# Kernel tuning notes

Hardware: AMD Instinct MI355X
Metric: run time of the kernel (lower is better)

## Reference

```python
import jax, jax.numpy as jnp
import numpy as np

B, S, H = 1, 2048, 4096
NH, NKV, HD = 32, 8, 128
N_REP = NH // NKV
SCALING = HD ** -0.5
ROPE_THETA = 10000.0
NEG_INF = -1e9


def setup_inputs() -> dict:
    key = jax.random.key(0)
    ks = jax.random.split(key, 5)
    hidden_states = jax.random.normal(ks[0], (B, S, H), dtype=jnp.float32)
    # torch nn.Linear weights are [out_features, in_features]
    wq = jax.random.normal(ks[1], (NH * HD, H), dtype=jnp.float32) * 0.02
    wk = jax.random.normal(ks[2], (NKV * HD, H), dtype=jnp.float32) * 0.02
    wv = jax.random.normal(ks[3], (NKV * HD, H), dtype=jnp.float32) * 0.02
    wo = jax.random.normal(ks[4], (NH * HD, H), dtype=jnp.float32).T * 0.02  # [H, NH*HD] -> store as [out,in]=[H,4096]
    wo = jnp.asarray(wo)
    # RoPE tables: [1, S, HD]
    inv_freq = 1.0 / (ROPE_THETA ** (jnp.arange(0, HD, 2, dtype=jnp.float32) / HD))
    pos = jnp.arange(S, dtype=jnp.float32)
    freqs = pos[:, None] * inv_freq[None, :]            # [S, HD/2]
    emb = jnp.concatenate([freqs, freqs], axis=-1)      # [S, HD]
    cos = jnp.cos(emb)[None]
    sin = jnp.sin(emb)[None]
    # additive causal mask [1, 1, S, S]
    causal = jnp.tril(jnp.ones((S, S), dtype=bool))
    attn_mask = jnp.where(causal, 0.0, NEG_INF).astype(jnp.float32)[None, None]
    return {"hidden_states": hidden_states, "wq": wq, "wk": wk, "wv": wv,
            "wo": wo, "cos": cos, "sin": sin, "attn_mask": attn_mask}


def rotate_half(x):
    x1, x2 = jnp.split(x, 2, axis=-1)
    return jnp.concatenate([-x2, x1], axis=-1)


def reference(hidden_states, wq, wk, wv, wo, cos, sin, attn_mask):
    b, s, _ = hidden_states.shape
    # projections (x @ W.T), reshape to [B, heads, S, HD]
    q = (hidden_states @ wq.T).reshape(b, s, NH, HD).transpose(0, 2, 1, 3)
    k = (hidden_states @ wk.T).reshape(b, s, NKV, HD).transpose(0, 2, 1, 3)
    v = (hidden_states @ wv.T).reshape(b, s, NKV, HD).transpose(0, 2, 1, 3)
    # RoPE (unsqueeze_dim=1)
    c = cos[:, None]  # [1,1,S,HD]
    sn = sin[:, None]
    q = q * c + rotate_half(q) * sn
    k = k * c + rotate_half(k) * sn
    # GQA head repeat
    k = jnp.repeat(k, N_REP, axis=1)  # [B, NH, S, HD]
    v = jnp.repeat(v, N_REP, axis=1)
    # eager attention
    scores = jnp.einsum('bhqd,bhkd->bhqk', q, k) * SCALING + attn_mask[:, :, :, :s]
    attn_weights = jax.nn.softmax(scores.astype(jnp.float32), axis=-1).astype(q.dtype)
    attn_out = jnp.einsum('bhqk,bhkd->bhqd', attn_weights, v)
    attn_out = attn_out.transpose(0, 2, 1, 3).reshape(b, s, NH * HD)
    out = attn_out @ wo.T
    return out, attn_weights
```

## Files before the change

### kernel.cpp

```cpp
#include <hip/hip_runtime.h>
#include <cstdint>
#include <cstddef>


#define SEQ 2048
#define HID 4096
#define NH_ 32
#define NKV_ 8
#define HD_ 128
#define KDIM_KV 1024
#define SCALING 0.08838834764831843f

typedef __bf16 bf16;
typedef __attribute__((ext_vector_type(8))) __bf16 bf16x8;
typedef __attribute__((ext_vector_type(4))) float f32x4;

__device__ __forceinline__ unsigned short f2bf(float f) {
  __bf16 h = (__bf16)f;
  return __builtin_bit_cast(unsigned short, h);
}
__device__ __forceinline__ float bf2f(unsigned short u) {
  unsigned int x = ((unsigned int)u) << 16;
  return __builtin_bit_cast(float, x);
}

__device__ __forceinline__ void async16(const void* g, void* l) {
  __builtin_amdgcn_global_load_lds(
      (const __attribute__((address_space(1))) unsigned int*)g,
      (__attribute__((address_space(3))) unsigned int*)l, 16, 0, 0);
}

__global__ __launch_bounds__(256) void cvt_kernel(const float* __restrict__ src,
                                                  bf16* __restrict__ dst, int n4) {
  int i = blockIdx.x * 256 + threadIdx.x;
  if (i >= n4) return;
  float4 v = ((const float4*)src)[i];
  union { unsigned short u[4]; uint2 vv; } pk;
  pk.u[0] = f2bf(v.x); pk.u[1] = f2bf(v.y);
  pk.u[2] = f2bf(v.z); pk.u[3] = f2bf(v.w);
  ((uint2*)dst)[i] = pk.vv;
}

__device__ __forceinline__ void gemm_mainloop(const char* Ab, const char* Bb,
                                              int K, char* smem, int tid,
                                              f32x4 (&acc)[4][4]) {
  const int wave = tid >> 6, lane = tid & 63;
  const int quad = lane >> 4, l16 = lane & 15;
  const int wm = wave >> 1, wn = wave & 1;
  bf16* As = (bf16*)smem;
  bf16* Bs = As + 128 * 32;

  const f32x4 fz = {0.f, 0.f, 0.f, 0.f};
#pragma unroll
  for (int i = 0; i < 4; i++)
#pragma unroll
    for (int j = 0; j < 4; j++) acc[i][j] = fz;

  const int o0 = (wave * 2 + 0) * 1024 + lane * 16;
  const int o1 = (wave * 2 + 1) * 1024 + lane * 16;
  const int rA0 = o0 >> 6, cA0 = o0 & 63;
  const int rA1 = o1 >> 6, cA1 = o1 & 63;

  for (int k0 = 0; k0 < K; k0 += 32) {
    __syncthreads();
    const size_t kb = (size_t)k0 * 2;
    async16(Ab + (size_t)rA0 * 8192 + kb + cA0, (char*)As + (wave * 2 + 0) * 1024);
    async16(Ab + (size_t)rA1 * 8192 + kb + cA1, (char*)As + (wave * 2 + 1) * 1024);
    async16(Bb + (size_t)rA0 * 8192 + kb + cA0, (char*)Bs + (wave * 2 + 0) * 1024);
    async16(Bb + (size_t)rA1 * 8192 + kb + cA1, (char*)Bs + (wave * 2 + 1) * 1024);
    __syncthreads();

    bf16x8 af[4], bfr[4];
#pragma unroll
    for (int i = 0; i < 4; i++)
      af[i] = *(const bf16x8*)(As + (size_t)(wm * 64 + i * 16 + l16) * 32 + quad * 8);
#pragma unroll
    for (int j = 0; j < 4; j++)
      bfr[j] = *(const bf16x8*)(Bs + (size_t)(wn * 64 + j * 16 + l16) * 32 + quad * 8);
#pragma unroll
    for (int i = 0; i < 4; i++)
#pragma unroll
      for (int j = 0; j < 4; j++)
        acc[i][j] = __builtin_amdgcn_mfma_f32_16x16x32_bf16(af[i], bfr[j], acc[i][j], 0, 0, 0);
  }
}

__global__ __launch_bounds__(256) void qkv_gemm(
    const bf16* __restrict__ A,
    const bf16* __restrict__ Wq,
    const bf16* __restrict__ Wk,
    const bf16* __restrict__ Wv,
    const float* __restrict__ cosp,
    const float* __restrict__ sinp,
    bf16* __restrict__ qout,
    bf16* __restrict__ kout,
    bf16* __restrict__ vtout)
{
  const int mi = blockIdx.x, nt = blockIdx.y;
  const int tid = threadIdx.x;
  const int wave = tid >> 6, lane = tid & 63;
  const int quad = lane >> 4, l16 = lane & 15;
  const int wm = wave >> 1, wn = wave & 1;

  const bf16* Bp; int nb;
  if (nt < 32)      { Bp = Wq; nb = nt; }
  else if (nt < 40) { Bp = Wk; nb = nt - 32; }
  else              { Bp = Wv; nb = nt - 40; }

  __shared__ __align__(16) char smem[128 * 132 * 4];

  f32x4 acc[4][4];
  gemm_mainloop((const char*)(A + (size_t)mi * 128 * HID),
                (const char*)(Bp + (size_t)nb * 128 * HID),
                HID, smem, tid, acc);

  __syncthreads();
  float* ct = (float*)smem;
#pragma unroll
  for (int i = 0; i < 4; i++)
#pragma unroll
    for (int j = 0; j < 4; j++)
#pragma unroll
      for (int r = 0; r < 4; r++)
        ct[(wm * 64 + i * 16 + quad * 4 + r) * 132 + wn * 64 + j * 16 + l16] = acc[i][j][r];
  __syncthreads();

  const int r0 = tid >> 4;
  const int c8 = (tid & 15) << 3;
  if (nt < 40) {
    bf16* outp; size_t ldo; int colbase;
    if (nt < 32) { outp = qout; ldo = HID; colbase = nt * 128; }
    else         { outp = kout; ldo = KDIM_KV; colbase = (nt - 32) * 128; }
#pragma unroll
    for (int p = 0; p < 8; p++) {
      int row = p * 16 + r0;
      int s = mi * 128 + row;
      union { unsigned short u[8]; uint4 v; } pk;
#pragma unroll
      for (int u8 = 0; u8 < 8; u8++) {
        int d = c8 + u8;
        float x  = ct[row * 132 + d];
        float xp = ct[row * 132 + (d ^ 64)];
        float cv = cosp[s * HD_ + d];
        float sv = sinp[s * HD_ + d];
        pk.u[u8] = f2bf(d < 64 ? x * cv - xp * sv : x * cv + xp * sv);
      }
      *(uint4*)(outp + (size_t)s * ldo + colbase + c8) = pk.v;
    }
  } else {
    int head = nt - 40;
#pragma unroll
    for (int p = 0; p < 8; p++) {
      int d = p * 16 + r0;
      union { unsigned short u[8]; uint4 v; } pk;
#pragma unroll
      for (int u8 = 0; u8 < 8; u8++)
        pk.u[u8] = f2bf(ct[(c8 + u8) * 132 + d]);
      *(uint4*)(vtout + ((size_t)head * HD_ + d) * SEQ + (size_t)mi * 128 + c8) = pk.v;
    }
  }
}

__device__ __forceinline__ void stage128(const bf16* __restrict__ base, int row_stride,
                                         unsigned short (*buf)[136], int tid) {
  const int r0 = tid >> 4;
  const int c = (tid & 15) * 8;
#pragma unroll
  for (int g = 0; g < 8; g++) {
    int row = g * 16 + r0;
    uint4 v = *(const uint4*)(base + (size_t)row * row_stride + c);
    *(uint4*)&buf[row][c] = v;
  }
}

__global__ __launch_bounds__(256, 3) void attn_kernel(
    const bf16* __restrict__ qb,
    const bf16* __restrict__ kb,
    const bf16* __restrict__ vtb,
    float* __restrict__ wout,
    bf16* __restrict__ aout)
{
  const int bid = blockIdx.x;
  const int h = bid & 31;
  const int qt = 31 - (bid >> 5);
  const int kvh = h >> 2;
  const int tid = threadIdx.x;
  const int wave = tid >> 6, lane = tid & 63;
  const int quad = lane >> 4, l16 = lane & 15;
  const int kmax = qt >> 1;

  __shared__ __align__(16) unsigned short kvbuf[128][136];
  __shared__ __align__(16) unsigned short wlds[64][136];

  {
    const int kc0 = (kmax + 1) * 128;
    if (kc0 < SEQ) {
      const float4 z = make_float4(0.f, 0.f, 0.f, 0.f);
      for (int row = 0; row < 64; row++) {
        float* zrow = wout + ((size_t)h * SEQ + (size_t)qt * 64 + row) * SEQ;
        for (int c = kc0 + (tid << 2); c < SEQ; c += 1024)
          *(float4*)(zrow + c) = z;
      }
    }
  }

  bf16x8 aq[4];
  {
    const bf16* qbase = qb + ((size_t)(qt * 64) + wave * 16 + l16) * HID + h * HD_;
#pragma unroll
    for (int ks = 0; ks < 4; ks++)
      aq[ks] = *(const bf16x8*)(qbase + ks * 32 + quad * 8);
  }

  float m_[4], l_[4];
#pragma unroll
  for (int r = 0; r < 4; r++) { m_[r] = -3.0e38f; l_[r] = 0.f; }

  for (int kt = 0; kt <= kmax; kt++) {
    __syncthreads();
    stage128(kb + (size_t)(kt * 128) * KDIM_KV + kvh * HD_, KDIM_KV, kvbuf, tid);
    __syncthreads();

    f32x4 acc[8];
    const f32x4 fz = {0.f, 0.f, 0.f, 0.f};
#pragma unroll
    for (int j = 0; j < 8; j++) acc[j] = fz;
#pragma unroll
    for (int ks = 0; ks < 4; ks++) {
      bf16x8 bk[8];
#pragma unroll
      for (int j = 0; j < 8; j++)
        bk[j] = *(const bf16x8*)&kvbuf[j * 16 + l16][ks * 32 + quad * 8];
#pragma unroll
      for (int j = 0; j < 8; j++)
        acc[j] = __builtin_amdgcn_mfma_f32_16x16x32_bf16(aq[ks], bk[j], acc[j], 0, 0, 0);
    }

    const bool mc = (kt == kmax);
#pragma unroll
    for (int r = 0; r < 4; r++) {
      int qrow = qt * 64 + wave * 16 + quad * 4 + r;
      float sv[8], mx = -3.0e38f;
#pragma unroll
      for (int j = 0; j < 8; j++) {
        float s = acc[j][r] * SCALING;
        if (mc && (kt * 128 + j * 16 + l16) > qrow) s -= 1.0e9f;
        sv[j] = s;
        mx = fmaxf(mx, s);
      }
#pragma unroll
      for (int sh = 1; sh < 16; sh <<= 1) mx = fmaxf(mx, __shfl_xor(mx, sh));
      float mn = fmaxf(m_[r], mx);
      float sum = 0.f;
#pragma unroll
      for (int j = 0; j < 8; j++) sum += __expf(sv[j] - mn);
#pragma unroll
      for (int sh = 1; sh < 16; sh <<= 1) sum += __shfl_xor(sum, sh);
      l_[r] = l_[r] * __expf(m_[r] - mn) + sum;
      m_[r] = mn;
    }
  }

  float linv[4];
#pragma unroll
  for (int r = 0; r < 4; r++) linv[r] = 1.f / l_[r];

  f32x4 oac[8];
  {
    const f32x4 fz = {0.f, 0.f, 0.f, 0.f};
#pragma unroll
    for (int j = 0; j < 8; j++) oac[j] = fz;
  }

  for (int kt = 0; kt <= kmax; kt++) {
    __syncthreads();
    stage128(kb + (size_t)(kt * 128) * KDIM_KV + kvh * HD_, KDIM_KV, kvbuf, tid);
    __syncthreads();

    f32x4 acc[8];
    const f32x4 fz = {0.f, 0.f, 0.f, 0.f};
#pragma unroll
    for (int j = 0; j < 8; j++) acc[j] = fz;
#pragma unroll
    for (int ks = 0; ks < 4; ks++) {
      bf16x8 bk[8];
#pragma unroll
      for (int j = 0; j < 8; j++)
        bk[j] = *(const bf16x8*)&kvbuf[j * 16 + l16][ks * 32 + quad * 8];
#pragma unroll
      for (int j = 0; j < 8; j++)
        acc[j] = __builtin_amdgcn_mfma_f32_16x16x32_bf16(aq[ks], bk[j], acc[j], 0, 0, 0);
    }

    const bool mc = (kt == kmax);
#pragma unroll
    for (int r = 0; r < 4; r++) {
      int qrow = qt * 64 + wave * 16 + quad * 4 + r;
#pragma unroll
      for (int j = 0; j < 8; j++) {
        float s = acc[j][r] * SCALING;
        if (mc && (kt * 128 + j * 16 + l16) > qrow) s -= 1.0e9f;
        wlds[wave * 16 + quad * 4 + r][j * 16 + l16] = f2bf(__expf(s - m_[r]) * linv[r]);
      }
    }
    __syncthreads();

    stage128(vtb + (size_t)kvh * HD_ * SEQ + kt * 128, SEQ, kvbuf, tid);
    {
      float* wdst = wout + ((size_t)h * SEQ + (size_t)qt * 64) * SEQ + kt * 128;
      const int rr = tid >> 5, c4 = (tid & 31) << 2;
#pragma unroll
      for (int p = 0; p < 8; p++) {
        int row = p * 8 + rr;
        uint2 w = *(const uint2*)&wlds[row][c4];
        float4 v;
        v.x = bf2f((unsigned short)(w.x & 0xffff));
        v.y = bf2f((unsigned short)(w.x >> 16));
        v.z = bf2f((unsigned short)(w.y & 0xffff));
        v.w = bf2f((unsigned short)(w.y >> 16));
        *(float4*)(wdst + (size_t)row * SEQ + c4) = v;
      }
    }
    __syncthreads();

#pragma unroll
    for (int ks = 0; ks < 4; ks++) {
      bf16x8 aw, bv[8];
      aw = *(const bf16x8*)&wlds[wave * 16 + l16][ks * 32 + quad * 8];
#pragma unroll
      for (int j = 0; j < 8; j++)
        bv[j] = *(const bf16x8*)&kvbuf[j * 16 + l16][ks * 32 + quad * 8];
#pragma unroll
      for (int j = 0; j < 8; j++)
        oac[j] = __builtin_amdgcn_mfma_f32_16x16x32_bf16(aw, bv[j], oac[j], 0, 0, 0);
    }
  }

  __syncthreads();
#pragma unroll
  for (int j = 0; j < 8; j++)
#pragma unroll
    for (int r = 0; r < 4; r++)
      wlds[wave * 16 + quad * 4 + r][j * 16 + l16] = f2bf(oac[j][r]);
  __syncthreads();
  {
    const int r0 = tid >> 4, c8 = (tid & 15) << 3;
    bf16* abase = aout + (size_t)(qt * 64) * HID + h * HD_;
#pragma unroll
    for (int p = 0; p < 4; p++) {
      int row = p * 16 + r0;
      union { unsigned short u[8]; uint4 v; } pk;
#pragma unroll
      for (int u8 = 0; u8 < 8; u8++) pk.u[u8] = wlds[row][c8 + u8];
      *(uint4*)(abase + (size_t)row * HID + c8) = pk.v;
    }
  }
}

__global__ __launch_bounds__(256) void proj_gemm(const bf16* __restrict__ A,
                                                 const bf16* __restrict__ B,
                                                 float* __restrict__ C) {
  const int mi = blockIdx.x, nt = blockIdx.y;
  const int tid = threadIdx.x;
  const int wave = tid >> 6, lane = tid & 63;
  const int quad = lane >> 4, l16 = lane & 15;
  const int wm = wave >> 1, wn = wave & 1;

  __shared__ __align__(16) char smem[16384];
  f32x4 acc[4][4];
  gemm_mainloop((const char*)(A + (size_t)mi * 128 * HID),
                (const char*)(B + (size_t)nt * 128 * HID),
                HID, smem, tid, acc);
#pragma unroll
  for (int i = 0; i < 4; i++)
#pragma unroll
    for (int j = 0; j < 4; j++)
#pragma unroll
      for (int r = 0; r < 4; r++) {
        int row = mi * 128 + wm * 64 + i * 16 + quad * 4 + r;
        int col = nt * 128 + wn * 64 + j * 16 + l16;
        C[(size_t)row * HID + col] = acc[i][j][r];
      }
}

extern "C" void kernel_launch(void* const* d_in, const int* in_sizes, int n_in,
                              void* d_out, int out_size, void* d_ws, size_t ws_size,
                              hipStream_t stream) {
  const float* hs   = (const float*)d_in[0];
  const float* wq   = (const float*)d_in[1];
  const float* wk   = (const float*)d_in[2];
  const float* wv   = (const float*)d_in[3];
  const float* wo   = (const float*)d_in[4];
  const float* cosp = (const float*)d_in[5];
  const float* sinp = (const float*)d_in[6];

  if (ws_size < (size_t)109051904) return;

  char* ws = (char*)d_ws;
  bf16* hsb = (bf16*)(ws + 0);
  bf16* wqb = (bf16*)(ws + 16777216);
  bf16* wkb = (bf16*)(ws + 50331648);
  bf16* wvb = (bf16*)(ws + 58720256);
  bf16* qb  = (bf16*)(ws + 67108864);
  bf16* kb  = (bf16*)(ws + 83886080);
  bf16* vtb = (bf16*)(ws + 88080384);
  bf16* aob = (bf16*)(ws + 92274688);

  float* outp = (float*)d_out;
  float* wout = outp + (size_t)SEQ * HID;

  cvt_kernel<<<2097152 / 256, 256, 0, stream>>>(hs, hsb, 2097152);
  cvt_kernel<<<4194304 / 256, 256, 0, stream>>>(wq, wqb, 4194304);
  cvt_kernel<<<1048576 / 256, 256, 0, stream>>>(wk, wkb, 1048576);
  cvt_kernel<<<1048576 / 256, 256, 0, stream>>>(wv, wvb, 1048576);

  qkv_gemm<<<dim3(16, 48), 256, 0, stream>>>(hsb, wqb, wkb, wvb, cosp, sinp, qb, kb, vtb);

  cvt_kernel<<<4194304 / 256, 256, 0, stream>>>(wo, wqb, 4194304);

  attn_kernel<<<1024, 256, 0, stream>>>(qb, kb, vtb, wout, aob);

  proj_gemm<<<dim3(16, 32), 256, 0, stream>>>(aob, wqb, outp);
}
```

Measured before the change: 1.143 ms.

## Rewrite projection GEMMs with 256-wide tiles and triple-buffered async LDS pipeline

Replaces the single-buffered 128x128 GEMM main loop with a 512-thread kernel using 256x256 (QKV) or 128x256 (output proj) tiles. Global-to-LDS loads go through a three-slot ring with explicit vmcnt waits, so loads for step t+2 overlap MFMA work on step t, and MFMA phases run at raised wave priority. The QKV epilogue is reworked to stage through LDS in 64-row chunks for RoPE and the V transpose. Larger tiles cut global traffic and barrier stalls per FLOP, but leave far fewer blocks (192 and 256) to spread over the GPU and need more LDS and registers.

```diff
diff --git a/kernel.cpp b/kernel.cpp
--- a/kernel.cpp
+++ b/kernel.cpp
@@ -41,51 +41,94 @@
   ((uint2*)dst)[i] = pk.vv;
 }
 
-__device__ __forceinline__ void gemm_mainloop(const char* Ab, const char* Bb,
-                                              int K, char* smem, int tid,
-                                              f32x4 (&acc)[4][4]) {
-  const int wave = tid >> 6, lane = tid & 63;
+template <int AR>
+__device__ __forceinline__ void gemm256_loop(const char* __restrict__ Ab,
+                                             const char* __restrict__ Bb,
+                                             char* smem,
+                                             f32x4 (&acc)[AR * 4][4]) {
+  const int NT = 128;
+  const int tid = threadIdx.x;
+  const int wid = tid >> 6, lane = tid & 63;
   const int quad = lane >> 4, l16 = lane & 15;
-  const int wm = wave >> 1, wn = wave & 1;
-  bf16* As = (bf16*)smem;
-  bf16* Bs = As + 128 * 32;
+  const int wm = wid >> 2, wn = wid & 3;
+  const int ASZ = AR * 8192;
+  const int SLOT = ASZ + 16384;
+
+  const char* gA0 = Ab + (size_t)(tid >> 2) * 8192 + (size_t)(tid & 3) * 16;
+  const char* gA1 = gA0 + (size_t)128 * 8192;
+  const char* gB0 = Bb + (size_t)(tid >> 2) * 8192 + (size_t)(tid & 3) * 16;
+  const char* gB1 = gB0 + (size_t)128 * 8192;
+  const int ldsA0 = wid * 1024;
+  const int ldsB0 = ASZ + wid * 1024;
 
   const f32x4 fz = {0.f, 0.f, 0.f, 0.f};
 #pragma unroll
-  for (int i = 0; i < 4; i++)
-#pragma unroll
-    for (int j = 0; j < 4; j++) acc[i][j] = fz;
-
-  const int o0 = (wave * 2 + 0) * 1024 + lane * 16;
-  const int o1 = (wave * 2 + 1) * 1024 + lane * 16;
-  const int rA0 = o0 >> 6, cA0 = o0 & 63;
-  const int rA1 = o1 >> 6, cA1 = o1 & 63;
-
-  for (int k0 = 0; k0 < K; k0 += 32) {
-    __syncthreads();
-    const size_t kb = (size_t)k0 * 2;
-    async16(Ab + (size_t)rA0 * 8192 + kb + cA0, (char*)As + (wave * 2 + 0) * 1024);
-    async16(Ab + (size_t)rA1 * 8192 + kb + cA1, (char*)As + (wave * 2 + 1) * 1024);
-    async16(Bb + (size_t)rA0 * 8192 + kb + cA0, (char*)Bs + (wave * 2 + 0) * 1024);
-    async16(Bb + (size_t)rA1 * 8192 + kb + cA1, (char*)Bs + (wave * 2 + 1) * 1024);
-    __syncthreads();
-
-    bf16x8 af[4], bfr[4];
-#pragma unroll
-    for (int i = 0; i < 4; i++)
-      af[i] = *(const bf16x8*)(As + (size_t)(wm * 64 + i * 16 + l16) * 32 + quad * 8);
-#pragma unroll
-    for (int j = 0; j < 4; j++)
-      bfr[j] = *(const bf16x8*)(Bs + (size_t)(wn * 64 + j * 16 + l16) * 32 + quad * 8);
-#pragma unroll
-    for (int i = 0; i < 4; i++)
-#pragma unroll
-      for (int j = 0; j < 4; j++)
-        acc[i][j] = __builtin_amdgcn_mfma_f32_16x16x32_bf16(af[i], bfr[j], acc[i][j], 0, 0, 0);
-  }
-}
-
-__global__ __launch_bounds__(256) void qkv_gemm(
+  for (int m = 0; m < AR * 4; m++)
+#pragma unroll
+    for (int n = 0; n < 4; n++) acc[m][n] = fz;
+
+#pragma unroll
+  for (int t = 0; t < 2; t++) {
+    char* sl = smem + t * SLOT;
+    async16(gA0 + t * 64, sl + ldsA0);
+    if (AR == 2) async16(gA1 + t * 64, sl + ldsA0 + 8192);
+    async16(gB0 + t * 64, sl + ldsB0);
+    async16(gB1 + t * 64, sl + ldsB0 + 8192);
+  }
+
+#pragma unroll 3
+  for (int t = 0; t < NT; t++) {
+    if (t + 1 < NT) {
+      if (AR == 2) asm volatile("s_waitcnt vmcnt(4)" ::: "memory");
+      else         asm volatile("s_waitcnt vmcnt(3)" ::: "memory");
+    } else {
+      asm volatile("s_waitcnt vmcnt(0)" ::: "memory");
+    }
+    __builtin_amdgcn_s_barrier();
+    __builtin_amdgcn_sched_barrier(0);
+    if (t + 2 < NT) {
+      char* sl = smem + ((t + 2) % 3) * SLOT;
+      async16(gA0 + (size_t)(t + 2) * 64, sl + ldsA0);
+      if (AR == 2) async16(gA1 + (size_t)(t + 2) * 64, sl + ldsA0 + 8192);
+    }
+    const bf16* sA = (const bf16*)(smem + (t % 3) * SLOT);
+    const bf16* sB = (const bf16*)(smem + (t % 3) * SLOT + ASZ);
+    bf16x8 a[AR * 2], b[4];
+#pragma unroll
+    for (int m = 0; m < AR * 2; m++)
+      a[m] = *(const bf16x8*)(sA + (size_t)(wm * (AR * 64) + m * 16 + l16) * 32 + quad * 8);
+#pragma unroll
+    for (int n = 0; n < 4; n++)
+      b[n] = *(const bf16x8*)(sB + (size_t)(wn * 64 + n * 16 + l16) * 32 + quad * 8);
+    __builtin_amdgcn_s_setprio(1);
+#pragma unroll
+    for (int m = 0; m < AR * 2; m++)
+#pragma unroll
+      for (int n = 0; n < 4; n++)
+        acc[m][n] = __builtin_amdgcn_mfma_f32_16x16x32_bf16(a[m], b[n], acc[m][n], 0, 0, 0);
+    __builtin_amdgcn_s_setprio(0);
+    __builtin_amdgcn_s_barrier();
+    __builtin_amdgcn_sched_barrier(0);
+    if (t + 2 < NT) {
+      char* sl = smem + ((t + 2) % 3) * SLOT;
+      async16(gB0 + (size_t)(t + 2) * 64, sl + ldsB0);
+      async16(gB1 + (size_t)(t + 2) * 64, sl + ldsB0 + 8192);
+    }
+#pragma unroll
+    for (int m = 0; m < AR * 2; m++)
+      a[m] = *(const bf16x8*)(sA + (size_t)(wm * (AR * 64) + (AR * 2 + m) * 16 + l16) * 32 + quad * 8);
+    __builtin_amdgcn_s_setprio(1);
+#pragma unroll
+    for (int m = 0; m < AR * 2; m++)
+#pragma unroll
+      for (int n = 0; n < 4; n++)
+        acc[AR * 2 + m][n] =
+            __builtin_amdgcn_mfma_f32_16x16x32_bf16(a[m], b[n], acc[AR * 2 + m][n], 0, 0, 0);
+    __builtin_amdgcn_s_setprio(0);
+  }
+}
+
+__global__ __launch_bounds__(512, 2) void qkv_gemm(
     const bf16* __restrict__ A,
     const bf16* __restrict__ Wq,
     const bf16* __restrict__ Wk,
@@ -96,68 +139,73 @@
     bf16* __restrict__ kout,
     bf16* __restrict__ vtout)
 {
+  extern __shared__ char smem[];
   const int mi = blockIdx.x, nt = blockIdx.y;
   const int tid = threadIdx.x;
-  const int wave = tid >> 6, lane = tid & 63;
+  const int wid = tid >> 6, lane = tid & 63;
   const int quad = lane >> 4, l16 = lane & 15;
-  const int wm = wave >> 1, wn = wave & 1;
-
-  const bf16* Bp; int nb;
-  if (nt < 32)      { Bp = Wq; nb = nt; }
-  else if (nt < 40) { Bp = Wk; nb = nt - 32; }
-  else              { Bp = Wv; nb = nt - 40; }
-
-  __shared__ __align__(16) char smem[128 * 132 * 4];
-
-  f32x4 acc[4][4];
-  gemm_mainloop((const char*)(A + (size_t)mi * 128 * HID),
-                (const char*)(Bp + (size_t)nb * 128 * HID),
-                HID, smem, tid, acc);
+  const int wm = wid >> 2, wn = wid & 3;
+
+  const bf16* Bp;
+  if (nt < 16)      Bp = Wq + (size_t)nt * 256 * HID;
+  else if (nt < 20) Bp = Wk + (size_t)(nt - 16) * 256 * HID;
+  else              Bp = Wv + (size_t)(nt - 20) * 256 * HID;
+
+  f32x4 acc[8][4];
+  gemm256_loop<2>((const char*)(A + (size_t)mi * 256 * HID), (const char*)Bp,
+                  smem, acc);
 
   __syncthreads();
   float* ct = (float*)smem;
-#pragma unroll
-  for (int i = 0; i < 4; i++)
-#pragma unroll
-    for (int j = 0; j < 4; j++)
-#pragma unroll
-      for (int r = 0; r < 4; r++)
-        ct[(wm * 64 + i * 16 + quad * 4 + r) * 132 + wn * 64 + j * 16 + l16] = acc[i][j][r];
-  __syncthreads();
-
-  const int r0 = tid >> 4;
-  const int c8 = (tid & 15) << 3;
-  if (nt < 40) {
-    bf16* outp; size_t ldo; int colbase;
-    if (nt < 32) { outp = qout; ldo = HID; colbase = nt * 128; }
-    else         { outp = kout; ldo = KDIM_KV; colbase = (nt - 32) * 128; }
-#pragma unroll
-    for (int p = 0; p < 8; p++) {
-      int row = p * 16 + r0;
-      int s = mi * 128 + row;
-      union { unsigned short u[8]; uint4 v; } pk;
-#pragma unroll
-      for (int u8 = 0; u8 < 8; u8++) {
-        int d = c8 + u8;
-        float x  = ct[row * 132 + d];
-        float xp = ct[row * 132 + (d ^ 64)];
-        float cv = cosp[s * HD_ + d];
-        float sv = sinp[s * HD_ + d];
-        pk.u[u8] = f2bf(d < 64 ? x * cv - xp * sv : x * cv + xp * sv);
-      }
-      *(uint4*)(outp + (size_t)s * ldo + colbase + c8) = pk.v;
-    }
-  } else {
-    int head = nt - 40;
-#pragma unroll
-    for (int p = 0; p < 8; p++) {
-      int d = p * 16 + r0;
-      union { unsigned short u[8]; uint4 v; } pk;
-#pragma unroll
-      for (int u8 = 0; u8 < 8; u8++)
-        pk.u[u8] = f2bf(ct[(c8 + u8) * 132 + d]);
-      *(uint4*)(vtout + ((size_t)head * HD_ + d) * SEQ + (size_t)mi * 128 + c8) = pk.v;
-    }
+  for (int ch = 0; ch < 4; ch++) {
+    if (wm == (ch >> 1)) {
+#pragma unroll
+      for (int mm = 0; mm < 4; mm++)
+#pragma unroll
+        for (int n = 0; n < 4; n++)
+#pragma unroll
+          for (int r = 0; r < 4; r++)
+            ct[(size_t)(mm * 16 + quad * 4 + r) * 265 + wn * 64 + n * 16 + l16] =
+                acc[(ch & 1) * 4 + mm][n][r];
+    }
+    __syncthreads();
+    if (nt < 20) {
+      const int r0 = tid >> 5, c8 = (tid & 31) << 3;
+      bf16* outp; int ldo, colbase;
+      if (nt < 16) { outp = qout; ldo = HID; colbase = nt * 256; }
+      else         { outp = kout; ldo = KDIM_KV; colbase = (nt - 16) * 256; }
+      const int d0 = c8 & 127;
+      const bool lo = d0 < 64;
+#pragma unroll
+      for (int p = 0; p < 4; p++) {
+        int row = p * 16 + r0;
+        int s = mi * 256 + ch * 64 + row;
+        union { unsigned short u[8]; uint4 v; } pk;
+#pragma unroll
+        for (int u8 = 0; u8 < 8; u8++) {
+          int c = c8 + u8;
+          float x  = ct[(size_t)row * 265 + c];
+          float xp = ct[(size_t)row * 265 + (c ^ 64)];
+          float cv = cosp[(size_t)s * HD_ + d0 + u8];
+          float sv = sinp[(size_t)s * HD_ + d0 + u8];
+          pk.u[u8] = f2bf(lo ? x * cv - xp * sv : x * cv + xp * sv);
+        }
+        *(uint4*)(outp + (size_t)s * ldo + colbase + c8) = pk.v;
+      }
+    } else {
+      const int dcol = tid & 255, sb = (tid >> 8) << 3;
+      const int vh = (nt - 20) * 2 + (dcol >> 7), dd = dcol & 127;
+#pragma unroll
+      for (int i = 0; i < 4; i++) {
+        int s8 = sb + i * 16;
+        union { unsigned short u[8]; uint4 v; } pk;
+#pragma unroll
+        for (int u8 = 0; u8 < 8; u8++)
+          pk.u[u8] = f2bf(ct[(size_t)(s8 + u8) * 265 + dcol]);
+        *(uint4*)(vtout + ((size_t)vh * HD_ + dd) * SEQ + mi * 256 + ch * 64 + s8) = pk.v;
+      }
+    }
+    __syncthreads();
   }
 }
 
@@ -357,29 +405,30 @@
   }
 }
 
-__global__ __launch_bounds__(256) void proj_gemm(const bf16* __restrict__ A,
-                                                 const bf16* __restrict__ B,
-                                                 float* __restrict__ C) {
+__global__ __launch_bounds__(512, 2) void proj_gemm(const bf16* __restrict__ A,
+                                                    const bf16* __restrict__ B,
+                                                    float* __restrict__ C) {
+  extern __shared__ char smem[];
   const int mi = blockIdx.x, nt = blockIdx.y;
   const int tid = threadIdx.x;
-  const int wave = tid >> 6, lane = tid & 63;
+  const int lane = tid & 63;
+  const int wid = tid >> 6;
   const int quad = lane >> 4, l16 = lane & 15;
-  const int wm = wave >> 1, wn = wave & 1;
-
-  __shared__ __align__(16) char smem[16384];
+  const int wm = wid >> 2, wn = wid & 3;
+
   f32x4 acc[4][4];
-  gemm_mainloop((const char*)(A + (size_t)mi * 128 * HID),
-                (const char*)(B + (size_t)nt * 128 * HID),
-                HID, smem, tid, acc);
-#pragma unroll
-  for (int i = 0; i < 4; i++)
-#pragma unroll
-    for (int j = 0; j < 4; j++)
+  gemm256_loop<1>((const char*)(A + (size_t)mi * 128 * HID),
+                  (const char*)(B + (size_t)nt * 256 * HID), smem, acc);
+
+#pragma unroll
+  for (int m = 0; m < 4; m++)
+#pragma unroll
+    for (int n = 0; n < 4; n++)
 #pragma unroll
       for (int r = 0; r < 4; r++) {
-        int row = mi * 128 + wm * 64 + i * 16 + quad * 4 + r;
-        int col = nt * 128 + wn * 64 + j * 16 + l16;
-        C[(size_t)row * HID + col] = acc[i][j][r];
+        int row = mi * 128 + wm * 64 + m * 16 + quad * 4 + r;
+        int col = nt * 256 + wn * 64 + n * 16 + l16;
+        C[(size_t)row * HID + col] = acc[m][n][r];
       }
 }
 
@@ -409,16 +458,21 @@
   float* outp = (float*)d_out;
   float* wout = outp + (size_t)SEQ * HID;
 
+  hipFuncSetAttribute((const void*)qkv_gemm,
+                      hipFuncAttributeMaxDynamicSharedMemorySize, 98304);
+  hipFuncSetAttribute((const void*)proj_gemm,
+                      hipFuncAttributeMaxDynamicSharedMemorySize, 73728);
+
   cvt_kernel<<<2097152 / 256, 256, 0, stream>>>(hs, hsb, 2097152);
   cvt_kernel<<<4194304 / 256, 256, 0, stream>>>(wq, wqb, 4194304);
   cvt_kernel<<<1048576 / 256, 256, 0, stream>>>(wk, wkb, 1048576);
   cvt_kernel<<<1048576 / 256, 256, 0, stream>>>(wv, wvb, 1048576);
 
-  qkv_gemm<<<dim3(16, 48), 256, 0, stream>>>(hsb, wqb, wkb, wvb, cosp, sinp, qb, kb, vtb);
+  qkv_gemm<<<dim3(8, 24), 512, 98304, stream>>>(hsb, wqb, wkb, wvb, cosp, sinp, qb, kb, vtb);
 
   cvt_kernel<<<4194304 / 256, 256, 0, stream>>>(wo, wqb, 4194304);
 
   attn_kernel<<<1024, 256, 0, stream>>>(qb, kb, vtb, wout, aob);
 
-  proj_gemm<<<dim3(16, 32), 256, 0, stream>>>(aob, wqb, outp);
-}
+  proj_gemm<<<dim3(16, 16), 512, 73728, stream>>>(aob, wqb, outp);
+}
```

After: 1.037 ms. -9.2%, faster.
